# Kernel optimization log

Measured on AMD Instinct MI355X. Metric: run time of the kernel, lower is better.

Reference implementation:

```python
import jax, jax.numpy as jnp
import numpy as np

B, LS, LL = 1024, 128, 2048
E, VOCAB = 16, 160000
NH, KD = 8, 6
LSH_DIM, TOPK = 16, 48
D_ITEM = 3 * E  # 48
EPS = 1e-3  # keras LayerNormalization default epsilon


def setup_inputs() -> dict:
    key = jax.random.key(0)
    ks = iter(jax.random.split(key, 64))
    def nk():
        return next(ks)
    def ids(shape):
        return jax.random.randint(nk(), shape, 0, VOCAB, dtype=jnp.int32)
    inp = {}
    for n in ['uid', 'utag1', 'utag2', 'utag3', 'utag4',
              'label_goods_ids', 'label_shop_ids', 'label_cate_ids']:
        inp[n] = ids((B,))
    for n in ['shortterm_goods_ids', 'shortterm_shop_ids', 'shortterm_cate_ids']:
        inp[n] = ids((B, LS))
    for n in ['longterm_goods_ids', 'longterm_shop_ids', 'longterm_cate_ids']:
        inp[n] = ids((B, LL))
    def rn(shape, s=0.05):
        return (jax.random.normal(nk(), shape) * s).astype(jnp.float32)
    inp['emb_table'] = rn((VOCAB, E))
    inp['H'] = rn((D_ITEM, LSH_DIM), 1.0)  # non-trainable random projection
    for p in ('s', 'l'):
        inp[p + 'Wq'] = rn((D_ITEM, NH, KD)); inp[p + 'bq'] = jnp.zeros((NH, KD), jnp.float32)
        inp[p + 'Wk'] = rn((D_ITEM, NH, KD)); inp[p + 'bk'] = jnp.zeros((NH, KD), jnp.float32)
        inp[p + 'Wv'] = rn((D_ITEM, NH, KD)); inp[p + 'bv'] = jnp.zeros((NH, KD), jnp.float32)
        inp[p + 'Wo'] = rn((NH, KD, D_ITEM)); inp[p + 'bo'] = jnp.zeros((D_ITEM,), jnp.float32)
    Din = D_ITEM + 5 * E + D_ITEM + D_ITEM  # 224
    inp['W1'] = rn((Din, 200)); inp['b1'] = jnp.zeros((200,), jnp.float32)
    inp['g1'] = jnp.ones((200,), jnp.float32); inp['be1'] = jnp.zeros((200,), jnp.float32)
    inp['W2'] = rn((200, 80)); inp['b2'] = jnp.zeros((80,), jnp.float32)
    inp['g2'] = jnp.ones((80,), jnp.float32); inp['be2'] = jnp.zeros((80,), jnp.float32)
    inp['W3'] = rn((80, 1)); inp['b3'] = jnp.zeros((1,), jnp.float32)
    return inp


def _ln(x, g, b):
    m = jnp.mean(x, axis=-1, keepdims=True)
    v = jnp.mean((x - m) ** 2, axis=-1, keepdims=True)
    return (x - m) * jax.lax.rsqrt(v + EPS) * g + b


def _mha(q, kv, mask3, Wq, bq, Wk, bk, Wv, bv, Wo, bo):
    # q: [B,1,D], kv: [B,K,D], mask3: [B,1,K] float (1=keep)
    qh = jnp.einsum('bqe,ehd->bqhd', q, Wq) + bq
    kh = jnp.einsum('bke,ehd->bkhd', kv, Wk) + bk
    vh = jnp.einsum('bke,ehd->bkhd', kv, Wv) + bv
    sc = jnp.einsum('bqhd,bkhd->bhqk', qh, kh) / jnp.sqrt(jnp.float32(KD))
    sc = sc + (1.0 - mask3[:, None, :, :]) * jnp.float32(-1e9)
    a = jax.nn.softmax(sc, axis=-1)
    o = jnp.einsum('bhqk,bkhd->bqhd', a, vh)
    return jnp.einsum('bqhd,hde->bqe', o, Wo) + bo


def reference(uid, utag1, utag2, utag3, utag4,
              label_goods_ids, label_shop_ids, label_cate_ids,
              shortterm_goods_ids, shortterm_shop_ids, shortterm_cate_ids,
              longterm_goods_ids, longterm_shop_ids, longterm_cate_ids,
              emb_table, H,
              sWq, sbq, sWk, sbk, sWv, sbv, sWo, sbo,
              lWq, lbq, lWk, lbk, lWv, lbv, lWo, lbo,
              W1, b1, g1, be1, W2, b2, g2, be2, W3, b3):
    short_mask = shortterm_goods_ids == 0  # padding_index == 0
    long_mask = longterm_goods_ids == 0

    def stack_embed(lst):
        X = jnp.stack([t if t.ndim == 2 else t[:, None] for t in lst], axis=2)  # [B,L,F]
        Xe = emb_table[X]  # [B,L,F,E]
        return Xe.reshape(Xe.shape[0], Xe.shape[1], -1)

    X_item = stack_embed([label_goods_ids, label_shop_ids, label_cate_ids])  # [B,1,48]
    X_user = stack_embed([uid, utag1, utag2, utag3, utag4])                  # [B,1,80]
    X_short = stack_embed([shortterm_goods_ids, shortterm_shop_ids, shortterm_cate_ids])  # [B,LS,48]
    X_long = stack_embed([longterm_goods_ids, longterm_shop_ids, longterm_cate_ids])      # [B,LL,48]

    # short-term interest
    slen = jnp.sum((~short_mask).astype(jnp.int32), axis=1)
    smask = (jnp.arange(LS)[None, :] < slen[:, None]).astype(jnp.float32)[:, None, :]
    short_int = _mha(X_item, X_short, smask, sWq, sbq, sWk, sbk, sWv, sbv, sWo, sbo)[:, 0]

    # long-term interest: LSH sign-hash hamming top-k retrieval
    series_codes = jnp.sign(jnp.einsum('ble,em->blm', X_long, H))  # [B,LL,16]
    item_codes = jnp.sign(jnp.einsum('ble,em->blm', X_item, H))    # [B,1,16]
    scores = jnp.sum((series_codes == item_codes).astype(jnp.float32), axis=-1)  # [B,LL]
    scores = jnp.where(long_mask, -jnp.inf, scores)
    _, idx = jax.lax.top_k(scores, TOPK)  # descending, padded entries last
    top_emb = jnp.take_along_axis(X_long, idx[:, :, None], axis=1)  # [B,TOPK,48]
    top_mask = jnp.take_along_axis(long_mask, idx, axis=1)
    llen = jnp.sum((~top_mask).astype(jnp.int32), axis=1)
    lmask = (jnp.arange(TOPK)[None, :] < llen[:, None]).astype(jnp.float32)[:, None, :]
    long_int = _mha(X_item, top_emb, lmask, lWq, lbq, lWk, lbk, lWv, lbv, lWo, lbo)[:, 0]

    x = jnp.concatenate([X_item[:, 0], X_user[:, 0], short_int, long_int], axis=1)  # [B,224]
    h1 = jax.nn.relu(_ln(x @ W1 + b1, g1, be1))
    h2 = jax.nn.relu(_ln(h1 @ W2 + b2, g2, be2))
    out = jax.nn.sigmoid(h2 @ W3 + b3)  # [B,1]
    return out
```

## Files before the change

### kernel.cpp

```cpp
#include <hip/hip_runtime.h>
#include <math.h>

#define BB 1024
#define LSx 128
#define LLx 2048
#define TOPKx 48

__global__ __launch_bounds__(256, 2) void k_score(
    const int* __restrict__ lg, const int* __restrict__ lsh, const int* __restrict__ lc,
    const int* __restrict__ ig, const int* __restrict__ ish, const int* __restrict__ ici,
    const float* __restrict__ emb, const float* __restrict__ Hm,
    signed char* __restrict__ gsc)
{
  __shared__ float Xitem[48];
  __shared__ int icode[16];
  __shared__ __align__(16) float4 xsh[256][5];
  const int b = blockIdx.y, tid = threadIdx.x;

  const int l = blockIdx.x * 256 + tid;
  const size_t off = (size_t)b * LLx + l;
  const int gid = lg[off];

  if (tid < 48) {
    const int seg = tid >> 4, e = tid & 15;
    const int id = (seg == 0) ? ig[b] : (seg == 1) ? ish[b] : ici[b];
    Xitem[tid] = emb[(size_t)id * 16 + e];
  }
  __syncthreads();
  if (tid < 16) {
    float dd = 0.f;
    for (int e = 0; e < 48; ++e) dd += Xitem[e] * Hm[e * 16 + tid];
    icode[tid] = (dd > 0.f) ? 1 : (dd < 0.f ? -1 : 0);
  }

  const int srow = tid >> 2;
  const int q = tid & 3;
  const size_t bbase = (size_t)b * LLx + (size_t)blockIdx.x * 256;

  float d[16];
  #pragma unroll
  for (int m = 0; m < 16; ++m) d[m] = 0.f;

  #pragma unroll
  for (int seg = 0; seg < 3; ++seg) {
    const int* idarr = (seg == 0) ? lg : (seg == 1) ? lsh : lc;
    #pragma unroll
    for (int jj = 0; jj < 4; ++jj) {
      const int pos = jj * 64 + srow;
      const int id = idarr[bbase + pos];
      xsh[pos][q] = *(const float4*)(emb + (size_t)id * 16 + q * 4);
    }
    __syncthreads();
    if (gid != 0) {
      float x[16];
      #pragma unroll
      for (int qq = 0; qq < 4; ++qq) {
        const float4 r = xsh[tid][qq];
        x[qq * 4 + 0] = r.x; x[qq * 4 + 1] = r.y;
        x[qq * 4 + 2] = r.z; x[qq * 4 + 3] = r.w;
      }
      const float* hb = Hm + seg * 256;
      #pragma unroll
      for (int i = 0; i < 16; ++i) {
        const float xi = x[i];
        #pragma unroll
        for (int mc = 0; mc < 4; ++mc) {
          const float4 h4 = *(const float4*)(hb + i * 16 + mc * 4);
          d[mc * 4 + 0] += xi * h4.x;
          d[mc * 4 + 1] += xi * h4.y;
          d[mc * 4 + 2] += xi * h4.z;
          d[mc * 4 + 3] += xi * h4.w;
        }
      }
    }
    if (seg < 2) __syncthreads();
  }

  int sc = -1;
  if (gid != 0) {
    sc = 0;
    #pragma unroll
    for (int m = 0; m < 16; ++m) {
      const int cs = (d[m] > 0.f) ? 1 : (d[m] < 0.f ? -1 : 0);
      sc += (cs == icode[m]) ? 1 : 0;
    }
  }
  gsc[off] = (signed char)sc;
}

__device__ __forceinline__ float block_sum256(float v, float* red) {
  #pragma unroll
  for (int m = 32; m >= 1; m >>= 1) v += __shfl_xor(v, m, 64);
  const int lane = threadIdx.x & 63, wave = threadIdx.x >> 6;
  if (lane == 0) red[wave] = v;
  __syncthreads();
  const float t = red[0] + red[1] + red[2] + red[3];
  __syncthreads();
  return t;
}

__global__ __launch_bounds__(256, 2) void k_fused(
    const int* __restrict__ sg, const int* __restrict__ ss, const int* __restrict__ scd,
    const int* __restrict__ lg, const int* __restrict__ ls, const int* __restrict__ lcd,
    const int* __restrict__ ig, const int* __restrict__ ish, const int* __restrict__ ici,
    const int* __restrict__ uid, const int* __restrict__ u1, const int* __restrict__ u2,
    const int* __restrict__ u3, const int* __restrict__ u4,
    const float* __restrict__ emb,
    const float* __restrict__ sWq, const float* __restrict__ sbq,
    const float* __restrict__ sWk, const float* __restrict__ sbk,
    const float* __restrict__ sWv, const float* __restrict__ sbv,
    const float* __restrict__ sWo, const float* __restrict__ sbo,
    const float* __restrict__ lWq, const float* __restrict__ lbq,
    const float* __restrict__ lWk, const float* __restrict__ lbk,
    const float* __restrict__ lWv, const float* __restrict__ lbv,
    const float* __restrict__ lWo, const float* __restrict__ lbo,
    const signed char* __restrict__ gsc,
    const float* __restrict__ W1, const float* __restrict__ b1,
    const float* __restrict__ g1, const float* __restrict__ be1,
    const float* __restrict__ W2, const float* __restrict__ b2,
    const float* __restrict__ g2, const float* __restrict__ be2,
    const float* __restrict__ W3, const float* __restrict__ b3,
    float* __restrict__ out)
{
  __shared__ float Xitem[48];
  __shared__ float qh_s[48], qh_l[48];
  __shared__ float vhs_sT[48][65];
  __shared__ float scs_s[8][LSx + 4];
  __shared__ float vhs_lT[48][TOPKx + 1];
  __shared__ float scs_l[8][TOPKx + 4];
  __shared__ float osm_s[48], osm_l[48];
  __shared__ unsigned char validf_s[LSx];
  __shared__ unsigned char validf_l[TOPKx];
  __shared__ int hist[18], wsum[4], nv[4], selsh[TOPKx];
  __shared__ int cnt_above;
  __shared__ __align__(16) float x[224];
  __shared__ __align__(16) float h1[200];
  __shared__ float h2[80];
  __shared__ float red[4];

  const int b = blockIdx.x, tid = threadIdx.x;
  const bool shorth = tid < 128;
  const int t = shorth ? tid : tid - 128;

  const int2 myv = ((const int2*)(gsc + (size_t)b * LLx))[tid];
  signed char loc[8];
  *(int2*)loc = myv;

  if (tid < 48) {
    const int seg = tid >> 4, e = tid & 15;
    const int id = (seg == 0) ? ig[b] : (seg == 1) ? ish[b] : ici[b];
    Xitem[tid] = emb[(size_t)id * 16 + e];
  }
  if (tid >= 160 && tid < 240) {
    const int u = tid - 160;
    const int f = u >> 4;
    const int id = (f == 0) ? uid[b] : (f == 1) ? u1[b] : (f == 2) ? u2[b]
                 : (f == 3) ? u3[b] : u4[b];
    x[48 + u] = emb[(size_t)id * 16 + (u & 15)];
  }
  if (tid < 18) hist[tid] = 0;
  if (tid == 0) cnt_above = 0;
  __syncthreads();

  #pragma unroll
  for (int j = 0; j < 8; ++j) atomicAdd(&hist[(int)loc[j] + 1], 1);
  if (tid < 48) {
    float a = sbq[tid];
    for (int e = 0; e < 48; ++e) a += Xitem[e] * sWq[e * 48 + tid];
    qh_s[tid] = a;
  } else if (tid >= 64 && tid < 112) {
    x[tid - 64] = Xitem[tid - 64];
  } else if (tid >= 128 && tid < 176) {
    float a = lbq[t];
    for (int e = 0; e < 48; ++e) a += Xitem[e] * lWq[e * 48 + t];
    qh_l[t] = a;
  }
  __syncthreads();

  int above = 0, tval = -1, need = 0;
  for (int s = 16; s >= -1; --s) {
    const int c = hist[s + 1];
    if (above + c >= TOPKx) { tval = s; need = TOPKx - above; break; }
    above += c;
  }
  const int base_l = tid * (LLx / 256);
  int cnt = 0;
  #pragma unroll
  for (int j = 0; j < 8; ++j) cnt += ((int)loc[j] == tval) ? 1 : 0;
  int v = cnt;
  const int lane = tid & 63, wave = tid >> 6;
  #pragma unroll
  for (int o = 1; o < 64; o <<= 1) {
    const int u = __shfl_up(v, o, 64);
    if (lane >= o) v += u;
  }
  if (lane == 63) wsum[wave] = v;
  __syncthreads();
  int rank = v - cnt;
  for (int w = 0; w < wave; ++w) rank += wsum[w];

  #pragma unroll
  for (int j = 0; j < 8; ++j) {
    const int l = base_l + j;
    const int s = (int)loc[j];
    if (s > tval) {
      const int slot = atomicAdd(&cnt_above, 1);
      selsh[slot] = l;
    } else if (s == tval) {
      if (rank < need) selsh[above + rank] = l;
      ++rank;
    }
  }
  __syncthreads();

  int gid = 0, sid = 0, cid = 0;
  if (shorth) {
    const size_t off = (size_t)b * LSx + t;
    gid = sg[off]; sid = ss[off]; cid = scd[off];
  } else if (t < TOPKx) {
    const int pos = selsh[t];
    const size_t off = (size_t)b * LLx + pos;
    gid = lg[off]; sid = ls[off]; cid = lcd[off];
  }
  const unsigned long long bal = __ballot(gid != 0);
  if ((tid & 63) == 0) nv[tid >> 6] = __popcll(bal);
  __syncthreads();
  const int nval = shorth ? (nv[0] + nv[1]) : (nv[2] + nv[3]);

  float vh[48];
  if (shorth) {
    validf_s[t] = (unsigned char)(t < nval);
    float kh[48];
    #pragma unroll
    for (int j = 0; j < 48; ++j) { kh[j] = sbk[j]; vh[j] = sbv[j]; }
    const int ids3[3] = {gid, sid, cid};
    #pragma unroll
    for (int seg = 0; seg < 3; ++seg) {
      const float* row = emb + (size_t)ids3[seg] * 16;
      #pragma unroll
      for (int i4 = 0; i4 < 4; ++i4) {
        const float4 xv = ((const float4*)row)[i4];
        const float xs[4] = {xv.x, xv.y, xv.z, xv.w};
        #pragma unroll
        for (int c = 0; c < 4; ++c) {
          const int e = seg * 16 + i4 * 4 + c;
          const float* wkr = sWk + e * 48;
          const float* wvr = sWv + e * 48;
          const float xe = xs[c];
          #pragma unroll
          for (int j = 0; j < 48; ++j) {
            kh[j] += xe * wkr[j];
            vh[j] += xe * wvr[j];
          }
        }
      }
    }
    #pragma unroll
    for (int h = 0; h < 8; ++h) {
      float s = 0.f;
      #pragma unroll
      for (int d = 0; d < 6; ++d) s += qh_s[h * 6 + d] * kh[h * 6 + d];
      scs_s[h][t] = s * 0.40824829046386301637f;
    }
    if (t < 64) {
      #pragma unroll
      for (int j = 0; j < 48; ++j) vhs_sT[j][t] = vh[j];
    }
  } else if (t < TOPKx) {
    validf_l[t] = (unsigned char)(gid != 0);
    float kh[48];
    #pragma unroll
    for (int j = 0; j < 48; ++j) { kh[j] = lbk[j]; vh[j] = lbv[j]; }
    const int ids3[3] = {gid, sid, cid};
    #pragma unroll
    for (int seg = 0; seg < 3; ++seg) {
      const float* row = emb + (size_t)ids3[seg] * 16;
      #pragma unroll
      for (int i4 = 0; i4 < 4; ++i4) {
        const float4 xv = ((const float4*)row)[i4];
        const float xs[4] = {xv.x, xv.y, xv.z, xv.w};
        #pragma unroll
        for (int c = 0; c < 4; ++c) {
          const int e = seg * 16 + i4 * 4 + c;
          const float* wkr = lWk + e * 48;
          const float* wvr = lWv + e * 48;
          const float xe = xs[c];
          #pragma unroll
          for (int j = 0; j < 48; ++j) {
            kh[j] += xe * wkr[j];
            vh[j] += xe * wvr[j];
          }
        }
      }
    }
    #pragma unroll
    for (int h = 0; h < 8; ++h) {
      float s = 0.f;
      #pragma unroll
      for (int d = 0; d < 6; ++d) s += qh_l[h * 6 + d] * kh[h * 6 + d];
      scs_l[h][t] = s * 0.40824829046386301637f;
    }
    #pragma unroll
    for (int j = 0; j < 48; ++j) vhs_lT[j][t] = vh[j];
  }
  __syncthreads();

  {
    const int h = t >> 4, l16 = t & 15;
    if (shorth) {
      float amax = -INFINITY;
      for (int k = l16; k < LSx; k += 16) if (validf_s[k]) amax = fmaxf(amax, scs_s[h][k]);
      #pragma unroll
      for (int m = 1; m < 16; m <<= 1) amax = fmaxf(amax, __shfl_xor(amax, m, 16));
      if (nval == 0) {
        for (int k = l16; k < LSx; k += 16) scs_s[h][k] = 1.0f / (float)LSx;
      } else {
        float ssum = 0.f;
        for (int k = l16; k < LSx; k += 16) {
          const float ev = validf_s[k] ? expf(scs_s[h][k] - amax) : 0.f;
          scs_s[h][k] = ev;
          ssum += ev;
        }
        #pragma unroll
        for (int m = 1; m < 16; m <<= 1) ssum += __shfl_xor(ssum, m, 16);
        const float inv = 1.0f / ssum;
        for (int k = l16; k < LSx; k += 16) scs_s[h][k] *= inv;
      }
    } else {
      float amax = -INFINITY;
      for (int k = l16; k < TOPKx; k += 16) if (validf_l[k]) amax = fmaxf(amax, scs_l[h][k]);
      #pragma unroll
      for (int m = 1; m < 16; m <<= 1) amax = fmaxf(amax, __shfl_xor(amax, m, 16));
      if (nval == 0) {
        for (int k = l16; k < TOPKx; k += 16) scs_l[h][k] = 1.0f / (float)TOPKx;
      } else {
        float ssum = 0.f;
        for (int k = l16; k < TOPKx; k += 16) {
          const float ev = validf_l[k] ? expf(scs_l[h][k] - amax) : 0.f;
          scs_l[h][k] = ev;
          ssum += ev;
        }
        #pragma unroll
        for (int m = 1; m < 16; m <<= 1) ssum += __shfl_xor(ssum, m, 16);
        const float inv = 1.0f / ssum;
        for (int k = l16; k < TOPKx; k += 16) scs_l[h][k] *= inv;
      }
    }
  }
  __syncthreads();

  float acc = 0.f;
  int hh = 0;
  if (tid < 48) {
    hh = tid / 6;
    for (int k = 0; k < 64; ++k) acc += scs_s[hh][k] * vhs_sT[tid][k];
  } else if (!shorth && t < 48) {
    const int h = t / 6;
    float a = 0.f;
    for (int k = 0; k < TOPKx; ++k) a += scs_l[h][k] * vhs_lT[t][k];
    osm_l[t] = a;
  }
  __syncthreads();

  if (shorth && t >= 64) {
    #pragma unroll
    for (int j = 0; j < 48; ++j) vhs_sT[j][t - 64] = vh[j];
  }
  __syncthreads();

  if (tid < 48) {
    for (int k = 64; k < LSx; ++k) acc += scs_s[hh][k] * vhs_sT[tid][k - 64];
    osm_s[tid] = acc;
  }
  __syncthreads();

  if (tid < 48) {
    float r = sbo[tid];
    for (int j = 0; j < 48; ++j) r += osm_s[j] * sWo[j * 48 + tid];
    x[128 + tid] = r;
  } else if (!shorth && t < 48) {
    float r = lbo[t];
    for (int j = 0; j < 48; ++j) r += osm_l[j] * lWo[j * 48 + t];
    x[176 + t] = r;
  }
  __syncthreads();

  float v1 = 0.f;
  if (tid < 200) {
    v1 = b1[tid];
    for (int i4 = 0; i4 < 56; ++i4) {
      const float4 xv = *(const float4*)(x + i4 * 4);
      const float* w = W1 + i4 * 4 * 200 + tid;
      v1 += xv.x * w[0];
      v1 += xv.y * w[200];
      v1 += xv.z * w[400];
      v1 += xv.w * w[600];
    }
  }
  const float mean1 = block_sum256((tid < 200) ? v1 : 0.f, red) * (1.0f / 200.0f);
  const float dv = (tid < 200) ? (v1 - mean1) : 0.f;
  const float var1 = block_sum256(dv * dv, red) * (1.0f / 200.0f);
  if (tid < 200) {
    const float y = (v1 - mean1) * rsqrtf(var1 + 1e-3f) * g1[tid] + be1[tid];
    h1[tid] = fmaxf(y, 0.f);
  }
  __syncthreads();

  float v2 = 0.f;
  if (tid < 80) {
    v2 = b2[tid];
    for (int i4 = 0; i4 < 50; ++i4) {
      const float4 xv = *(const float4*)(h1 + i4 * 4);
      const float* w = W2 + i4 * 4 * 80 + tid;
      v2 += xv.x * w[0];
      v2 += xv.y * w[80];
      v2 += xv.z * w[160];
      v2 += xv.w * w[240];
    }
  }
  const float mean2 = block_sum256((tid < 80) ? v2 : 0.f, red) * (1.0f / 80.0f);
  const float dv2 = (tid < 80) ? (v2 - mean2) : 0.f;
  const float var2 = block_sum256(dv2 * dv2, red) * (1.0f / 80.0f);
  if (tid < 80) {
    const float y = (v2 - mean2) * rsqrtf(var2 + 1e-3f) * g2[tid] + be2[tid];
    h2[tid] = fmaxf(y, 0.f);
  }
  __syncthreads();

  const float p = (tid < 80) ? h2[tid] * W3[tid] : 0.f;
  const float z = block_sum256(p, red);
  if (tid == 0) {
    out[b] = 1.0f / (1.0f + expf(-(z + b3[0])));
  }
}

extern "C" void kernel_launch(void* const* d_in, const int* in_sizes, int n_in,
                              void* d_out, int out_size, void* d_ws, size_t ws_size,
                              hipStream_t stream) {
  (void)in_sizes; (void)n_in; (void)out_size; (void)ws_size;
  const int* uid = (const int*)d_in[0];
  const int* u1  = (const int*)d_in[1];
  const int* u2  = (const int*)d_in[2];
  const int* u3  = (const int*)d_in[3];
  const int* u4  = (const int*)d_in[4];
  const int* ig  = (const int*)d_in[5];
  const int* ish = (const int*)d_in[6];
  const int* ici = (const int*)d_in[7];
  const int* sg  = (const int*)d_in[8];
  const int* ss  = (const int*)d_in[9];
  const int* scd = (const int*)d_in[10];
  const int* lg  = (const int*)d_in[11];
  const int* ls  = (const int*)d_in[12];
  const int* lcd = (const int*)d_in[13];
  const float* emb = (const float*)d_in[14];
  const float* Hm  = (const float*)d_in[15];
  const float* sWq = (const float*)d_in[16];
  const float* sbq = (const float*)d_in[17];
  const float* sWk = (const float*)d_in[18];
  const float* sbk = (const float*)d_in[19];
  const float* sWv = (const float*)d_in[20];
  const float* sbv = (const float*)d_in[21];
  const float* sWo = (const float*)d_in[22];
  const float* sbo = (const float*)d_in[23];
  const float* lWq = (const float*)d_in[24];
  const float* lbq = (const float*)d_in[25];
  const float* lWk = (const float*)d_in[26];
  const float* lbk = (const float*)d_in[27];
  const float* lWv = (const float*)d_in[28];
  const float* lbv = (const float*)d_in[29];
  const float* lWo = (const float*)d_in[30];
  const float* lbo = (const float*)d_in[31];
  const float* W1 = (const float*)d_in[32];
  const float* b1 = (const float*)d_in[33];
  const float* g1 = (const float*)d_in[34];
  const float* be1 = (const float*)d_in[35];
  const float* W2 = (const float*)d_in[36];
  const float* b2 = (const float*)d_in[37];
  const float* g2 = (const float*)d_in[38];
  const float* be2 = (const float*)d_in[39];
  const float* W3 = (const float*)d_in[40];
  const float* b3 = (const float*)d_in[41];
  float* out = (float*)d_out;

  signed char* gsc = (signed char*)d_ws;

  k_score<<<dim3(LLx / 256, BB), dim3(256), 0, stream>>>(
      lg, ls, lcd, ig, ish, ici, emb, Hm, gsc);
  k_fused<<<dim3(BB), dim3(256), 0, stream>>>(
      sg, ss, scd, lg, ls, lcd, ig, ish, ici,
      uid, u1, u2, u3, u4, emb,
      sWq, sbq, sWk, sbk, sWv, sbv, sWo, sbo,
      lWq, lbq, lWk, lbk, lWv, lbv, lWo, lbo,
      gsc,
      W1, b1, g1, be1, W2, b2, g2, be2, W3, b3, out);
}
```

Baseline: 328.2 us.

## Move short-term attention into the scoring kernel as interleaved blocks

The short-term MHA branch moves out of the second kernel and into the LSH scoring launch. Every ninth block of a 1D grid handles one batch row's short attention, and the other eight blocks score long-sequence chunks. The short-term result goes through a workspace buffer to the second kernel, which now does only top-k, long attention and the MLP. The aim is to run the short-attention work concurrently with the memory-bound scoring and make the serial second kernel shorter. In exchange it adds a global round-trip for 48 floats per row, and the union of shared-memory layouts may affect occupancy.

```diff
diff --git a/kernel.cpp b/kernel.cpp
--- a/kernel.cpp
+++ b/kernel.cpp
@@ -6,230 +6,136 @@
 #define LLx 2048
 #define TOPKx 48
 
-__global__ __launch_bounds__(256, 2) void k_score(
+struct SmemScore {
+  float4 xsh[256][5];
+  float Xitem[48];
+  int icode[16];
+};
+struct SmemShort {
+  float vhsT[48][65];
+  float scs[8][LSx + 4];
+  float Xitem[48];
+  float qh[48];
+  float osm[48];
+  unsigned char validf[LSx];
+};
+
+__global__ __launch_bounds__(256, 2) void k_score_short(
     const int* __restrict__ lg, const int* __restrict__ lsh, const int* __restrict__ lc,
+    const int* __restrict__ sg, const int* __restrict__ ss, const int* __restrict__ scd,
     const int* __restrict__ ig, const int* __restrict__ ish, const int* __restrict__ ici,
     const float* __restrict__ emb, const float* __restrict__ Hm,
-    signed char* __restrict__ gsc)
-{
-  __shared__ float Xitem[48];
-  __shared__ int icode[16];
-  __shared__ __align__(16) float4 xsh[256][5];
-  const int b = blockIdx.y, tid = threadIdx.x;
-
-  const int l = blockIdx.x * 256 + tid;
-  const size_t off = (size_t)b * LLx + l;
-  const int gid = lg[off];
-
-  if (tid < 48) {
-    const int seg = tid >> 4, e = tid & 15;
-    const int id = (seg == 0) ? ig[b] : (seg == 1) ? ish[b] : ici[b];
-    Xitem[tid] = emb[(size_t)id * 16 + e];
-  }
-  __syncthreads();
-  if (tid < 16) {
-    float dd = 0.f;
-    for (int e = 0; e < 48; ++e) dd += Xitem[e] * Hm[e * 16 + tid];
-    icode[tid] = (dd > 0.f) ? 1 : (dd < 0.f ? -1 : 0);
-  }
-
-  const int srow = tid >> 2;
-  const int q = tid & 3;
-  const size_t bbase = (size_t)b * LLx + (size_t)blockIdx.x * 256;
-
-  float d[16];
-  #pragma unroll
-  for (int m = 0; m < 16; ++m) d[m] = 0.f;
-
-  #pragma unroll
-  for (int seg = 0; seg < 3; ++seg) {
-    const int* idarr = (seg == 0) ? lg : (seg == 1) ? lsh : lc;
-    #pragma unroll
-    for (int jj = 0; jj < 4; ++jj) {
-      const int pos = jj * 64 + srow;
-      const int id = idarr[bbase + pos];
-      xsh[pos][q] = *(const float4*)(emb + (size_t)id * 16 + q * 4);
-    }
-    __syncthreads();
-    if (gid != 0) {
-      float x[16];
-      #pragma unroll
-      for (int qq = 0; qq < 4; ++qq) {
-        const float4 r = xsh[tid][qq];
-        x[qq * 4 + 0] = r.x; x[qq * 4 + 1] = r.y;
-        x[qq * 4 + 2] = r.z; x[qq * 4 + 3] = r.w;
-      }
-      const float* hb = Hm + seg * 256;
-      #pragma unroll
-      for (int i = 0; i < 16; ++i) {
-        const float xi = x[i];
-        #pragma unroll
-        for (int mc = 0; mc < 4; ++mc) {
-          const float4 h4 = *(const float4*)(hb + i * 16 + mc * 4);
-          d[mc * 4 + 0] += xi * h4.x;
-          d[mc * 4 + 1] += xi * h4.y;
-          d[mc * 4 + 2] += xi * h4.z;
-          d[mc * 4 + 3] += xi * h4.w;
-        }
-      }
-    }
-    if (seg < 2) __syncthreads();
-  }
-
-  int sc = -1;
-  if (gid != 0) {
-    sc = 0;
-    #pragma unroll
-    for (int m = 0; m < 16; ++m) {
-      const int cs = (d[m] > 0.f) ? 1 : (d[m] < 0.f ? -1 : 0);
-      sc += (cs == icode[m]) ? 1 : 0;
-    }
-  }
-  gsc[off] = (signed char)sc;
-}
-
-__device__ __forceinline__ float block_sum256(float v, float* red) {
-  #pragma unroll
-  for (int m = 32; m >= 1; m >>= 1) v += __shfl_xor(v, m, 64);
-  const int lane = threadIdx.x & 63, wave = threadIdx.x >> 6;
-  if (lane == 0) red[wave] = v;
-  __syncthreads();
-  const float t = red[0] + red[1] + red[2] + red[3];
-  __syncthreads();
-  return t;
-}
-
-__global__ __launch_bounds__(256, 2) void k_fused(
-    const int* __restrict__ sg, const int* __restrict__ ss, const int* __restrict__ scd,
-    const int* __restrict__ lg, const int* __restrict__ ls, const int* __restrict__ lcd,
-    const int* __restrict__ ig, const int* __restrict__ ish, const int* __restrict__ ici,
-    const int* __restrict__ uid, const int* __restrict__ u1, const int* __restrict__ u2,
-    const int* __restrict__ u3, const int* __restrict__ u4,
-    const float* __restrict__ emb,
     const float* __restrict__ sWq, const float* __restrict__ sbq,
     const float* __restrict__ sWk, const float* __restrict__ sbk,
     const float* __restrict__ sWv, const float* __restrict__ sbv,
     const float* __restrict__ sWo, const float* __restrict__ sbo,
-    const float* __restrict__ lWq, const float* __restrict__ lbq,
-    const float* __restrict__ lWk, const float* __restrict__ lbk,
-    const float* __restrict__ lWv, const float* __restrict__ lbv,
-    const float* __restrict__ lWo, const float* __restrict__ lbo,
-    const signed char* __restrict__ gsc,
-    const float* __restrict__ W1, const float* __restrict__ b1,
-    const float* __restrict__ g1, const float* __restrict__ be1,
-    const float* __restrict__ W2, const float* __restrict__ b2,
-    const float* __restrict__ g2, const float* __restrict__ be2,
-    const float* __restrict__ W3, const float* __restrict__ b3,
-    float* __restrict__ out)
+    signed char* __restrict__ gsc, float* __restrict__ sint)
 {
-  __shared__ float Xitem[48];
-  __shared__ float qh_s[48], qh_l[48];
-  __shared__ float vhs_sT[48][65];
-  __shared__ float scs_s[8][LSx + 4];
-  __shared__ float vhs_lT[48][TOPKx + 1];
-  __shared__ float scs_l[8][TOPKx + 4];
-  __shared__ float osm_s[48], osm_l[48];
-  __shared__ unsigned char validf_s[LSx];
-  __shared__ unsigned char validf_l[TOPKx];
-  __shared__ int hist[18], wsum[4], nv[4], selsh[TOPKx];
-  __shared__ int cnt_above;
-  __shared__ __align__(16) float x[224];
-  __shared__ __align__(16) float h1[200];
-  __shared__ float h2[80];
-  __shared__ float red[4];
-
-  const int b = blockIdx.x, tid = threadIdx.x;
-  const bool shorth = tid < 128;
-  const int t = shorth ? tid : tid - 128;
-
-  const int2 myv = ((const int2*)(gsc + (size_t)b * LLx))[tid];
-  signed char loc[8];
-  *(int2*)loc = myv;
+  __shared__ union { SmemScore a; SmemShort m; } sm;
+  const int bid = blockIdx.x, tid = threadIdx.x;
+
+  if (bid % 9 != 0) {
+    const int idx = bid - bid / 9 - 1;
+    const int b = idx >> 3;
+    const int chunk = idx & 7;
+
+    const int l = chunk * 256 + tid;
+    const size_t off = (size_t)b * LLx + l;
+    const int gid = lg[off];
+
+    if (tid < 48) {
+      const int seg = tid >> 4, e = tid & 15;
+      const int id = (seg == 0) ? ig[b] : (seg == 1) ? ish[b] : ici[b];
+      sm.a.Xitem[tid] = emb[(size_t)id * 16 + e];
+    }
+    __syncthreads();
+    if (tid < 16) {
+      float dd = 0.f;
+      for (int e = 0; e < 48; ++e) dd += sm.a.Xitem[e] * Hm[e * 16 + tid];
+      sm.a.icode[tid] = (dd > 0.f) ? 1 : (dd < 0.f ? -1 : 0);
+    }
+
+    const int srow = tid >> 2;
+    const int q = tid & 3;
+    const size_t bbase = (size_t)b * LLx + (size_t)chunk * 256;
+
+    float d[16];
+    #pragma unroll
+    for (int m = 0; m < 16; ++m) d[m] = 0.f;
+
+    #pragma unroll
+    for (int seg = 0; seg < 3; ++seg) {
+      const int* idarr = (seg == 0) ? lg : (seg == 1) ? lsh : lc;
+      #pragma unroll
+      for (int jj = 0; jj < 4; ++jj) {
+        const int pos = jj * 64 + srow;
+        const int id = idarr[bbase + pos];
+        sm.a.xsh[pos][q] = *(const float4*)(emb + (size_t)id * 16 + q * 4);
+      }
+      __syncthreads();
+      if (gid != 0) {
+        float x[16];
+        #pragma unroll
+        for (int qq = 0; qq < 4; ++qq) {
+          const float4 r = sm.a.xsh[tid][qq];
+          x[qq * 4 + 0] = r.x; x[qq * 4 + 1] = r.y;
+          x[qq * 4 + 2] = r.z; x[qq * 4 + 3] = r.w;
+        }
+        const float* hb = Hm + seg * 256;
+        #pragma unroll
+        for (int i = 0; i < 16; ++i) {
+          const float xi = x[i];
+          #pragma unroll
+          for (int mc = 0; mc < 4; ++mc) {
+            const float4 h4 = *(const float4*)(hb + i * 16 + mc * 4);
+            d[mc * 4 + 0] += xi * h4.x;
+            d[mc * 4 + 1] += xi * h4.y;
+            d[mc * 4 + 2] += xi * h4.z;
+            d[mc * 4 + 3] += xi * h4.w;
+          }
+        }
+      }
+      if (seg < 2) __syncthreads();
+    }
+
+    int sc = -1;
+    if (gid != 0) {
+      sc = 0;
+      #pragma unroll
+      for (int m = 0; m < 16; ++m) {
+        const int cs = (d[m] > 0.f) ? 1 : (d[m] < 0.f ? -1 : 0);
+        sc += (cs == sm.a.icode[m]) ? 1 : 0;
+      }
+    }
+    gsc[off] = (signed char)sc;
+    return;
+  }
+
+  const int b = bid / 9;
+  const int t = tid;
 
   if (tid < 48) {
     const int seg = tid >> 4, e = tid & 15;
     const int id = (seg == 0) ? ig[b] : (seg == 1) ? ish[b] : ici[b];
-    Xitem[tid] = emb[(size_t)id * 16 + e];
-  }
-  if (tid >= 160 && tid < 240) {
-    const int u = tid - 160;
-    const int f = u >> 4;
-    const int id = (f == 0) ? uid[b] : (f == 1) ? u1[b] : (f == 2) ? u2[b]
-                 : (f == 3) ? u3[b] : u4[b];
-    x[48 + u] = emb[(size_t)id * 16 + (u & 15)];
-  }
-  if (tid < 18) hist[tid] = 0;
-  if (tid == 0) cnt_above = 0;
-  __syncthreads();
-
-  #pragma unroll
-  for (int j = 0; j < 8; ++j) atomicAdd(&hist[(int)loc[j] + 1], 1);
+    sm.m.Xitem[tid] = emb[(size_t)id * 16 + e];
+  }
+  __syncthreads();
   if (tid < 48) {
     float a = sbq[tid];
-    for (int e = 0; e < 48; ++e) a += Xitem[e] * sWq[e * 48 + tid];
-    qh_s[tid] = a;
-  } else if (tid >= 64 && tid < 112) {
-    x[tid - 64] = Xitem[tid - 64];
-  } else if (tid >= 128 && tid < 176) {
-    float a = lbq[t];
-    for (int e = 0; e < 48; ++e) a += Xitem[e] * lWq[e * 48 + t];
-    qh_l[t] = a;
-  }
-  __syncthreads();
-
-  int above = 0, tval = -1, need = 0;
-  for (int s = 16; s >= -1; --s) {
-    const int c = hist[s + 1];
-    if (above + c >= TOPKx) { tval = s; need = TOPKx - above; break; }
-    above += c;
-  }
-  const int base_l = tid * (LLx / 256);
-  int cnt = 0;
-  #pragma unroll
-  for (int j = 0; j < 8; ++j) cnt += ((int)loc[j] == tval) ? 1 : 0;
-  int v = cnt;
-  const int lane = tid & 63, wave = tid >> 6;
-  #pragma unroll
-  for (int o = 1; o < 64; o <<= 1) {
-    const int u = __shfl_up(v, o, 64);
-    if (lane >= o) v += u;
-  }
-  if (lane == 63) wsum[wave] = v;
-  __syncthreads();
-  int rank = v - cnt;
-  for (int w = 0; w < wave; ++w) rank += wsum[w];
-
-  #pragma unroll
-  for (int j = 0; j < 8; ++j) {
-    const int l = base_l + j;
-    const int s = (int)loc[j];
-    if (s > tval) {
-      const int slot = atomicAdd(&cnt_above, 1);
-      selsh[slot] = l;
-    } else if (s == tval) {
-      if (rank < need) selsh[above + rank] = l;
-      ++rank;
-    }
-  }
-  __syncthreads();
+    for (int e = 0; e < 48; ++e) a += sm.m.Xitem[e] * sWq[e * 48 + tid];
+    sm.m.qh[tid] = a;
+  }
 
   int gid = 0, sid = 0, cid = 0;
-  if (shorth) {
+  if (tid < 128) {
     const size_t off = (size_t)b * LSx + t;
     gid = sg[off]; sid = ss[off]; cid = scd[off];
-  } else if (t < TOPKx) {
-    const int pos = selsh[t];
-    const size_t off = (size_t)b * LLx + pos;
-    gid = lg[off]; sid = ls[off]; cid = lcd[off];
-  }
-  const unsigned long long bal = __ballot(gid != 0);
-  if ((tid & 63) == 0) nv[tid >> 6] = __popcll(bal);
-  __syncthreads();
-  const int nval = shorth ? (nv[0] + nv[1]) : (nv[2] + nv[3]);
+  }
+  const int nval = __syncthreads_count((tid < 128) && (gid != 0));
 
   float vh[48];
-  if (shorth) {
-    validf_s[t] = (unsigned char)(t < nval);
+  if (tid < 128) {
+    sm.m.validf[t] = (unsigned char)(t < nval);
     float kh[48];
     #pragma unroll
     for (int j = 0; j < 48; ++j) { kh[j] = sbk[j]; vh[j] = sbv[j]; }
@@ -259,16 +165,186 @@
     for (int h = 0; h < 8; ++h) {
       float s = 0.f;
       #pragma unroll
-      for (int d = 0; d < 6; ++d) s += qh_s[h * 6 + d] * kh[h * 6 + d];
-      scs_s[h][t] = s * 0.40824829046386301637f;
+      for (int d2 = 0; d2 < 6; ++d2) s += sm.m.qh[h * 6 + d2] * kh[h * 6 + d2];
+      sm.m.scs[h][t] = s * 0.40824829046386301637f;
     }
     if (t < 64) {
       #pragma unroll
-      for (int j = 0; j < 48; ++j) vhs_sT[j][t] = vh[j];
-    }
-  } else if (t < TOPKx) {
-    validf_l[t] = (unsigned char)(gid != 0);
-    float kh[48];
+      for (int j = 0; j < 48; ++j) sm.m.vhsT[j][t] = vh[j];
+    }
+  }
+  __syncthreads();
+
+  if (tid < 128) {
+    const int h = t >> 4, l16 = t & 15;
+    float amax = -INFINITY;
+    for (int k = l16; k < LSx; k += 16) if (sm.m.validf[k]) amax = fmaxf(amax, sm.m.scs[h][k]);
+    #pragma unroll
+    for (int m = 1; m < 16; m <<= 1) amax = fmaxf(amax, __shfl_xor(amax, m, 16));
+    if (nval == 0) {
+      for (int k = l16; k < LSx; k += 16) sm.m.scs[h][k] = 1.0f / (float)LSx;
+    } else {
+      float ssum = 0.f;
+      for (int k = l16; k < LSx; k += 16) {
+        const float ev = sm.m.validf[k] ? expf(sm.m.scs[h][k] - amax) : 0.f;
+        sm.m.scs[h][k] = ev;
+        ssum += ev;
+      }
+      #pragma unroll
+      for (int m = 1; m < 16; m <<= 1) ssum += __shfl_xor(ssum, m, 16);
+      const float inv = 1.0f / ssum;
+      for (int k = l16; k < LSx; k += 16) sm.m.scs[h][k] *= inv;
+    }
+  }
+  __syncthreads();
+
+  float acc = 0.f;
+  int hh = 0;
+  if (tid < 48) {
+    hh = tid / 6;
+    for (int k = 0; k < 64; ++k) acc += sm.m.scs[hh][k] * sm.m.vhsT[tid][k];
+  }
+  __syncthreads();
+  if (tid >= 64 && tid < 128) {
+    #pragma unroll
+    for (int j = 0; j < 48; ++j) sm.m.vhsT[j][t - 64] = vh[j];
+  }
+  __syncthreads();
+  if (tid < 48) {
+    for (int k = 64; k < LSx; ++k) acc += sm.m.scs[hh][k] * sm.m.vhsT[tid][k - 64];
+    sm.m.osm[tid] = acc;
+  }
+  __syncthreads();
+  if (tid < 48) {
+    float r = sbo[tid];
+    for (int j = 0; j < 48; ++j) r += sm.m.osm[j] * sWo[j * 48 + tid];
+    sint[b * 48 + tid] = r;
+  }
+}
+
+__device__ __forceinline__ float block_sum256(float v, float* red) {
+  #pragma unroll
+  for (int m = 32; m >= 1; m >>= 1) v += __shfl_xor(v, m, 64);
+  const int lane = threadIdx.x & 63, wave = threadIdx.x >> 6;
+  if (lane == 0) red[wave] = v;
+  __syncthreads();
+  const float t = red[0] + red[1] + red[2] + red[3];
+  __syncthreads();
+  return t;
+}
+
+__global__ __launch_bounds__(256, 2) void k_long_mlp(
+    const int* __restrict__ lg, const int* __restrict__ ls, const int* __restrict__ lcd,
+    const int* __restrict__ ig, const int* __restrict__ ish, const int* __restrict__ ici,
+    const int* __restrict__ uid, const int* __restrict__ u1, const int* __restrict__ u2,
+    const int* __restrict__ u3, const int* __restrict__ u4,
+    const float* __restrict__ emb,
+    const float* __restrict__ lWq, const float* __restrict__ lbq,
+    const float* __restrict__ lWk, const float* __restrict__ lbk,
+    const float* __restrict__ lWv, const float* __restrict__ lbv,
+    const float* __restrict__ lWo, const float* __restrict__ lbo,
+    const signed char* __restrict__ gsc, const float* __restrict__ sint,
+    const float* __restrict__ W1, const float* __restrict__ b1,
+    const float* __restrict__ g1, const float* __restrict__ be1,
+    const float* __restrict__ W2, const float* __restrict__ b2,
+    const float* __restrict__ g2, const float* __restrict__ be2,
+    const float* __restrict__ W3, const float* __restrict__ b3,
+    float* __restrict__ out)
+{
+  __shared__ float Xitem[48];
+  __shared__ float qh_l[48];
+  __shared__ float vhs_lT[48][TOPKx + 1];
+  __shared__ float scs_l[8][TOPKx + 4];
+  __shared__ float osm_l[48];
+  __shared__ unsigned char validf_l[TOPKx];
+  __shared__ int hist[18], wsum[4], selsh[TOPKx];
+  __shared__ int cnt_above;
+  __shared__ __align__(16) float x[224];
+  __shared__ __align__(16) float h1[200];
+  __shared__ float h2[80];
+  __shared__ float red[4];
+
+  const int b = blockIdx.x, tid = threadIdx.x;
+
+  const int2 myv = ((const int2*)(gsc + (size_t)b * LLx))[tid];
+  signed char loc[8];
+  *(int2*)loc = myv;
+
+  if (tid < 48) {
+    const int seg = tid >> 4, e = tid & 15;
+    const int id = (seg == 0) ? ig[b] : (seg == 1) ? ish[b] : ici[b];
+    Xitem[tid] = emb[(size_t)id * 16 + e];
+  } else if (tid >= 112 && tid < 160) {
+    x[128 + (tid - 112)] = sint[b * 48 + (tid - 112)];
+  } else if (tid >= 160 && tid < 240) {
+    const int u = tid - 160;
+    const int f = u >> 4;
+    const int id = (f == 0) ? uid[b] : (f == 1) ? u1[b] : (f == 2) ? u2[b]
+                 : (f == 3) ? u3[b] : u4[b];
+    x[48 + u] = emb[(size_t)id * 16 + (u & 15)];
+  }
+  if (tid < 18) hist[tid] = 0;
+  if (tid == 0) cnt_above = 0;
+  __syncthreads();
+
+  #pragma unroll
+  for (int j = 0; j < 8; ++j) atomicAdd(&hist[(int)loc[j] + 1], 1);
+  if (tid < 48) {
+    float a = lbq[tid];
+    for (int e = 0; e < 48; ++e) a += Xitem[e] * lWq[e * 48 + tid];
+    qh_l[tid] = a;
+  } else if (tid >= 64 && tid < 112) {
+    x[tid - 64] = Xitem[tid - 64];
+  }
+  __syncthreads();
+
+  int above = 0, tval = -1, need = 0;
+  for (int s = 16; s >= -1; --s) {
+    const int c = hist[s + 1];
+    if (above + c >= TOPKx) { tval = s; need = TOPKx - above; break; }
+    above += c;
+  }
+  const int base_l = tid * (LLx / 256);
+  int cnt = 0;
+  #pragma unroll
+  for (int j = 0; j < 8; ++j) cnt += ((int)loc[j] == tval) ? 1 : 0;
+  int v = cnt;
+  const int lane = tid & 63, wave = tid >> 6;
+  #pragma unroll
+  for (int o = 1; o < 64; o <<= 1) {
+    const int u = __shfl_up(v, o, 64);
+    if (lane >= o) v += u;
+  }
+  if (lane == 63) wsum[wave] = v;
+  __syncthreads();
+  int rank = v - cnt;
+  for (int w = 0; w < wave; ++w) rank += wsum[w];
+
+  #pragma unroll
+  for (int j = 0; j < 8; ++j) {
+    const int l = base_l + j;
+    const int s = (int)loc[j];
+    if (s > tval) {
+      const int slot = atomicAdd(&cnt_above, 1);
+      selsh[slot] = l;
+    } else if (s == tval) {
+      if (rank < need) selsh[above + rank] = l;
+      ++rank;
+    }
+  }
+  __syncthreads();
+
+  int gid = 0, sid = 0, cid = 0;
+  if (tid < TOPKx) {
+    const int pos = selsh[tid];
+    const size_t off = (size_t)b * LLx + pos;
+    gid = lg[off]; sid = ls[off]; cid = lcd[off];
+  }
+  const int nval = __syncthreads_count((tid < TOPKx) && (gid != 0));
+
+  if (tid < TOPKx) {
+    validf_l[tid] = (unsigned char)(gid != 0);
+    float kh[48], vh[48];
     #pragma unroll
     for (int j = 0; j < 48; ++j) { kh[j] = lbk[j]; vh[j] = lbv[j]; }
     const int ids3[3] = {gid, sid, cid};
@@ -297,91 +373,49 @@
     for (int h = 0; h < 8; ++h) {
       float s = 0.f;
       #pragma unroll
-      for (int d = 0; d < 6; ++d) s += qh_l[h * 6 + d] * kh[h * 6 + d];
-      scs_l[h][t] = s * 0.40824829046386301637f;
-    }
-    #pragma unroll
-    for (int j = 0; j < 48; ++j) vhs_lT[j][t] = vh[j];
-  }
-  __syncthreads();
-
-  {
-    const int h = t >> 4, l16 = t & 15;
-    if (shorth) {
-      float amax = -INFINITY;
-      for (int k = l16; k < LSx; k += 16) if (validf_s[k]) amax = fmaxf(amax, scs_s[h][k]);
-      #pragma unroll
-      for (int m = 1; m < 16; m <<= 1) amax = fmaxf(amax, __shfl_xor(amax, m, 16));
-      if (nval == 0) {
-        for (int k = l16; k < LSx; k += 16) scs_s[h][k] = 1.0f / (float)LSx;
-      } else {
-        float ssum = 0.f;
-        for (int k = l16; k < LSx; k += 16) {
-          const float ev = validf_s[k] ? expf(scs_s[h][k] - amax) : 0.f;
-          scs_s[h][k] = ev;
-          ssum += ev;
-        }
-        #pragma unroll
-        for (int m = 1; m < 16; m <<= 1) ssum += __shfl_xor(ssum, m, 16);
-        const float inv = 1.0f / ssum;
-        for (int k = l16; k < LSx; k += 16) scs_s[h][k] *= inv;
-      }
+      for (int d2 = 0; d2 < 6; ++d2) s += qh_l[h * 6 + d2] * kh[h * 6 + d2];
+      scs_l[h][tid] = s * 0.40824829046386301637f;
+    }
+    #pragma unroll
+    for (int j = 0; j < 48; ++j) vhs_lT[j][tid] = vh[j];
+  }
+  __syncthreads();
+
+  if (tid < 128) {
+    const int h = tid >> 4, l16 = tid & 15;
+    float amax = -INFINITY;
+    for (int k = l16; k < TOPKx; k += 16) if (validf_l[k]) amax = fmaxf(amax, scs_l[h][k]);
+    #pragma unroll
+    for (int m = 1; m < 16; m <<= 1) amax = fmaxf(amax, __shfl_xor(amax, m, 16));
+    if (nval == 0) {
+      for (int k = l16; k < TOPKx; k += 16) scs_l[h][k] = 1.0f / (float)TOPKx;
     } else {
-      float amax = -INFINITY;
-      for (int k = l16; k < TOPKx; k += 16) if (validf_l[k]) amax = fmaxf(amax, scs_l[h][k]);
-      #pragma unroll
-      for (int m = 1; m < 16; m <<= 1) amax = fmaxf(amax, __shfl_xor(amax, m, 16));
-      if (nval == 0) {
-        for (int k = l16; k < TOPKx; k += 16) scs_l[h][k] = 1.0f / (float)TOPKx;
-      } else {
-        float ssum = 0.f;
-        for (int k = l16; k < TOPKx; k += 16) {
-          const float ev = validf_l[k] ? expf(scs_l[h][k] - amax) : 0.f;
-          scs_l[h][k] = ev;
-          ssum += ev;
-        }
-        #pragma unroll
-        for (int m = 1; m < 16; m <<= 1) ssum += __shfl_xor(ssum, m, 16);
-        const float inv = 1.0f / ssum;
-        for (int k = l16; k < TOPKx; k += 16) scs_l[h][k] *= inv;
-      }
-    }
-  }
-  __syncthreads();
-
-  float acc = 0.f;
-  int hh = 0;
-  if (tid < 48) {
-    hh = tid / 6;
-    for (int k = 0; k < 64; ++k) acc += scs_s[hh][k] * vhs_sT[tid][k];
-  } else if (!shorth && t < 48) {
-    const int h = t / 6;
+      float ssum = 0.f;
+      for (int k = l16; k < TOPKx; k += 16) {
+        const float ev = validf_l[k] ? expf(scs_l[h][k] - amax) : 0.f;
+        scs_l[h][k] = ev;
+        ssum += ev;
+      }
+      #pragma unroll
+      for (int m = 1; m < 16; m <<= 1) ssum += __shfl_xor(ssum, m, 16);
+      const float inv = 1.0f / ssum;
+      for (int k = l16; k < TOPKx; k += 16) scs_l[h][k] *= inv;
+    }
+  }
+  __syncthreads();
+
+  if (tid < 48) {
+    const int h = tid / 6;
     float a = 0.f;
-    for (int k = 0; k < TOPKx; ++k) a += scs_l[h][k] * vhs_lT[t][k];
-    osm_l[t] = a;
-  }
-  __syncthreads();
-
-  if (shorth && t >= 64) {
-    #pragma unroll
-    for (int j = 0; j < 48; ++j) vhs_sT[j][t - 64] = vh[j];
-  }
-  __syncthreads();
-
-  if (tid < 48) {
-    for (int k = 64; k < LSx; ++k) acc += scs_s[hh][k] * vhs_sT[tid][k - 64];
-    osm_s[tid] = acc;
-  }
-  __syncthreads();
-
-  if (tid < 48) {
-    float r = sbo[tid];
-    for (int j = 0; j < 48; ++j) r += osm_s[j] * sWo[j * 48 + tid];
-    x[128 + tid] = r;
-  } else if (!shorth && t < 48) {
-    float r = lbo[t];
-    for (int j = 0; j < 48; ++j) r += osm_l[j] * lWo[j * 48 + t];
-    x[176 + t] = r;
+    for (int k = 0; k < TOPKx; ++k) a += scs_l[h][k] * vhs_lT[tid][k];
+    osm_l[tid] = a;
+  }
+  __syncthreads();
+
+  if (tid < 48) {
+    float r = lbo[tid];
+    for (int j = 0; j < 48; ++j) r += osm_l[j] * lWo[j * 48 + tid];
+    x[176 + tid] = r;
   }
   __syncthreads();
 
@@ -483,14 +517,15 @@
   float* out = (float*)d_out;
 
   signed char* gsc = (signed char*)d_ws;
-
-  k_score<<<dim3(LLx / 256, BB), dim3(256), 0, stream>>>(
-      lg, ls, lcd, ig, ish, ici, emb, Hm, gsc);
-  k_fused<<<dim3(BB), dim3(256), 0, stream>>>(
-      sg, ss, scd, lg, ls, lcd, ig, ish, ici,
+  float* sint = (float*)((char*)d_ws + (size_t)BB * LLx);
+
+  k_score_short<<<dim3(9216), dim3(256), 0, stream>>>(
+      lg, ls, lcd, sg, ss, scd, ig, ish, ici, emb, Hm,
+      sWq, sbq, sWk, sbk, sWv, sbv, sWo, sbo, gsc, sint);
+  k_long_mlp<<<dim3(BB), dim3(256), 0, stream>>>(
+      lg, ls, lcd, ig, ish, ici,
       uid, u1, u2, u3, u4, emb,
-      sWq, sbq, sWk, sbk, sWv, sbv, sWo, sbo,
       lWq, lbq, lWk, lbk, lWv, lbv, lWo, lbo,
-      gsc,
+      gsc, sint,
       W1, b1, g1, be1, W2, b2, g2, be2, W3, b3, out);
 }
```

After: 385.5 us. +17.5%, slower.
